# Performance work log

Hardware: AMD Instinct MI355X
Metric: run time of the kernel (lower is better)

Reference implementation:

```python
import jax, jax.numpy as jnp
import numpy as np

EPS = 1e-8  # epsilon from padded_softmax


def setup_inputs() -> dict:
    key = jax.random.key(0)
    k1, k2 = jax.random.split(key)
    B, N, NC = 32, 1024, 3
    C = jax.random.normal(k1, (B, N, NC), dtype=jnp.float32)
    masks = jnp.ones((B, N, N), dtype=jnp.float32)
    # nn.Parameter(torch.rand(1) * 0.02 + 0.99)
    inverse_sigma = jax.random.uniform(k2, (1,), dtype=jnp.float32) * 0.02 + 0.99
    return {"C": C, "masks": masks, "inverse_sigma": inverse_sigma}


def reference(C, masks, inverse_sigma):
    # Pairwise squared euclidean distances via the Gram-matrix identity
    # ||x-y||^2 = ||x||^2 + ||y||^2 - 2<x,y>  (avoids the [B,N,N,NC] expand).
    sq = jnp.sum(C * C, axis=-1)                                  # [B, N]
    gram = jnp.einsum('bnc,bmc->bnm', C, C)                       # [B, N, N]
    D = sq[:, :, None] + sq[:, None, :] - 2.0 * gram              # [B, N, N]
    # Gaussian kernel adjacency.
    A = jnp.exp(-(inverse_sigma ** 2) * D)                        # [B, N, N]
    # padded_softmax: exp(-A) * masks, normalized along last axis.
    X = jnp.exp(-A) * masks
    return X / (jnp.sum(X, axis=-1, keepdims=True) + EPS)
```

## Files before the change

### kernel.cpp

```cpp
#include <hip/hip_runtime.h>

#define EPS 1e-8f
#define LOG2E 1.4426950408889634f

typedef float f32x4 __attribute__((ext_vector_type(4)));

__global__ __launch_bounds__(256) void gaussian_rownorm_kernel(
    const float* __restrict__ C,
    const float* __restrict__ masks,
    const float* __restrict__ inv_sigma,
    float* __restrict__ out,
    int N)
{
    const int n   = blockIdx.x;
    const int b   = blockIdx.y;
    const int t   = threadIdx.x;

    const float s  = inv_sigma[0];
    const float k1 = -(s * s) * LOG2E;

    const float* __restrict__ Cb = C + (size_t)b * N * 3;

    const float cn0 = Cb[n * 3 + 0];
    const float cn1 = Cb[n * 3 + 1];
    const float cn2 = Cb[n * 3 + 2];
    const float sqn = cn0 * cn0 + cn1 * cn1 + cn2 * cn2;

    const int m0 = t * 4;
    const f32x4* __restrict__ cm = (const f32x4*)(Cb + (size_t)m0 * 3);
    const f32x4 ca  = cm[0];
    const f32x4 cb4 = cm[1];
    const f32x4 cc  = cm[2];

    const size_t rowbase = ((size_t)b * N + n) * N;
    const f32x4 mk = __builtin_nontemporal_load((const f32x4*)(masks + rowbase + m0));

    #define CALC(c0, c1, c2, mval)                                   \
        ({                                                           \
            float _sqm = (c0)*(c0) + (c1)*(c1) + (c2)*(c2);          \
            float _dot = cn0*(c0) + cn1*(c1) + cn2*(c2);             \
            float _D   = sqn + _sqm - 2.0f * _dot;                   \
            float _A   = __builtin_amdgcn_exp2f(k1 * _D);            \
            __builtin_amdgcn_exp2f(-LOG2E * _A) * (mval);            \
        })

    const float x0 = CALC(ca.x,  ca.y,  ca.z,  mk.x);
    const float x1 = CALC(ca.w,  cb4.x, cb4.y, mk.y);
    const float x2 = CALC(cb4.z, cb4.w, cc.x,  mk.z);
    const float x3 = CALC(cc.y,  cc.z,  cc.w,  mk.w);
    #undef CALC

    float psum = (x0 + x1) + (x2 + x3);
    #pragma unroll
    for (int off = 32; off > 0; off >>= 1)
        psum += __shfl_xor(psum, off, 64);

    __shared__ float wsum[4];
    const int wid = t >> 6;
    if ((t & 63) == 0) wsum[wid] = psum;
    __syncthreads();

    const float total = wsum[0] + wsum[1] + wsum[2] + wsum[3];
    const float r = 1.0f / (total + EPS);

    f32x4 o;
    o.x = x0 * r; o.y = x1 * r; o.z = x2 * r; o.w = x3 * r;
    __builtin_nontemporal_store(o, (f32x4*)(out + rowbase + m0));
}

extern "C" void kernel_launch(void* const* d_in, const int* in_sizes, int n_in,
                              void* d_out, int out_size, void* d_ws, size_t ws_size,
                              hipStream_t stream) {
    const float* C         = (const float*)d_in[0];
    const float* masks     = (const float*)d_in[1];
    const float* inv_sigma = (const float*)d_in[2];
    float* out             = (float*)d_out;

    const long long N_ll = (long long)out_size * 3LL / (long long)in_sizes[0];
    const int N = (int)N_ll;
    const int B = in_sizes[0] / (3 * N);

    const int block = N / 4;
    dim3 grid(N, B);

    gaussian_rownorm_kernel<<<grid, block, 0, stream>>>(C, masks, inv_sigma, out, N);
}
```

Baseline: 231.0 us.

## Map one wavefront per row for N=1024 to drop block-level reduction

Adds a specialized kernel for N=1024 in which each 64-lane wavefront handles a whole row, with each lane processing 16 elements. The row sum is then done with wavefront shuffles only, removing the shared-memory write and __syncthreads, and each block covers four rows, which cuts the block count by four. All four mask loads are issued up front to raise memory-level parallelism. The trade-off is more registers per thread and a shape-specialized path, with the old kernel kept as a fallback for other sizes.

```diff
diff --git a/kernel.cpp b/kernel.cpp
--- a/kernel.cpp
+++ b/kernel.cpp
@@ -5,22 +5,92 @@
 
 typedef float f32x4 __attribute__((ext_vector_type(4)));
 
-__global__ __launch_bounds__(256) void gaussian_rownorm_kernel(
+#define CALC(c0, c1, c2, mval, cn0, cn1, cn2, sqn, k1)           \
+    ({                                                           \
+        float _sqm = (c0)*(c0) + (c1)*(c1) + (c2)*(c2);          \
+        float _dot = (cn0)*(c0) + (cn1)*(c1) + (cn2)*(c2);       \
+        float _D   = (sqn) + _sqm - 2.0f * _dot;                 \
+        float _A   = __builtin_amdgcn_exp2f((k1) * _D);          \
+        __builtin_amdgcn_exp2f(-LOG2E * _A) * (mval);            \
+    })
+
+__global__ __launch_bounds__(256) void gaussian_rownorm_1024(
+    const float* __restrict__ C,
+    const float* __restrict__ masks,
+    const float* __restrict__ inv_sigma,
+    float* __restrict__ out)
+{
+    constexpr int N = 1024;
+    const int wid  = threadIdx.x >> 6;
+    const int lane = threadIdx.x & 63;
+    const int row  = blockIdx.x * 4 + wid;
+    const int b    = row >> 10;
+    const int n    = row & (N - 1);
+
+    const float s  = inv_sigma[0];
+    const float k1 = -(s * s) * LOG2E;
+
+    const float* __restrict__ Cb = C + (size_t)b * N * 3;
+    const float cn0 = Cb[n * 3 + 0];
+    const float cn1 = Cb[n * 3 + 1];
+    const float cn2 = Cb[n * 3 + 2];
+    const float sqn = cn0 * cn0 + cn1 * cn1 + cn2 * cn2;
+
+    const size_t rowbase = (size_t)row * N;
+
+    f32x4 mk[4];
+    #pragma unroll
+    for (int k = 0; k < 4; ++k)
+        mk[k] = __builtin_nontemporal_load(
+            (const f32x4*)(masks + rowbase + k * 256 + lane * 4));
+
+    float x[16];
+    float psum = 0.0f;
+    #pragma unroll
+    for (int k = 0; k < 4; ++k) {
+        const int m0 = k * 256 + lane * 4;
+        const f32x4* __restrict__ cm = (const f32x4*)(Cb + m0 * 3);
+        const f32x4 ca  = cm[0];
+        const f32x4 cb4 = cm[1];
+        const f32x4 cc  = cm[2];
+
+        x[k*4+0] = CALC(ca.x,  ca.y,  ca.z,  mk[k].x, cn0, cn1, cn2, sqn, k1);
+        x[k*4+1] = CALC(ca.w,  cb4.x, cb4.y, mk[k].y, cn0, cn1, cn2, sqn, k1);
+        x[k*4+2] = CALC(cb4.z, cb4.w, cc.x,  mk[k].z, cn0, cn1, cn2, sqn, k1);
+        x[k*4+3] = CALC(cc.y,  cc.z,  cc.w,  mk[k].w, cn0, cn1, cn2, sqn, k1);
+        psum += (x[k*4+0] + x[k*4+1]) + (x[k*4+2] + x[k*4+3]);
+    }
+
+    #pragma unroll
+    for (int off = 32; off > 0; off >>= 1)
+        psum += __shfl_xor(psum, off, 64);
+
+    const float r = 1.0f / (psum + EPS);
+
+    #pragma unroll
+    for (int k = 0; k < 4; ++k) {
+        f32x4 o;
+        o.x = x[k*4+0] * r; o.y = x[k*4+1] * r;
+        o.z = x[k*4+2] * r; o.w = x[k*4+3] * r;
+        __builtin_nontemporal_store(o, (f32x4*)(out + rowbase + k * 256 + lane * 4));
+    }
+}
+
+__global__ __launch_bounds__(256) void gaussian_rownorm_generic(
     const float* __restrict__ C,
     const float* __restrict__ masks,
     const float* __restrict__ inv_sigma,
     float* __restrict__ out,
     int N)
 {
-    const int n   = blockIdx.x;
-    const int b   = blockIdx.y;
-    const int t   = threadIdx.x;
+    const int n = blockIdx.x;
+    const int b = blockIdx.y;
+    const int t = threadIdx.x;
 
     const float s  = inv_sigma[0];
     const float k1 = -(s * s) * LOG2E;
 
     const float* __restrict__ Cb = C + (size_t)b * N * 3;
-
     const float cn0 = Cb[n * 3 + 0];
     const float cn1 = Cb[n * 3 + 1];
     const float cn2 = Cb[n * 3 + 2];
@@ -35,20 +105,10 @@
     const size_t rowbase = ((size_t)b * N + n) * N;
     const f32x4 mk = __builtin_nontemporal_load((const f32x4*)(masks + rowbase + m0));
 
-    #define CALC(c0, c1, c2, mval)                                   \
-        ({                                                           \
-            float _sqm = (c0)*(c0) + (c1)*(c1) + (c2)*(c2);          \
-            float _dot = cn0*(c0) + cn1*(c1) + cn2*(c2);             \
-            float _D   = sqn + _sqm - 2.0f * _dot;                   \
-            float _A   = __builtin_amdgcn_exp2f(k1 * _D);            \
-            __builtin_amdgcn_exp2f(-LOG2E * _A) * (mval);            \
-        })
-
-    const float x0 = CALC(ca.x,  ca.y,  ca.z,  mk.x);
-    const float x1 = CALC(ca.w,  cb4.x, cb4.y, mk.y);
-    const float x2 = CALC(cb4.z, cb4.w, cc.x,  mk.z);
-    const float x3 = CALC(cc.y,  cc.z,  cc.w,  mk.w);
-    #undef CALC
+    const float x0 = CALC(ca.x,  ca.y,  ca.z,  mk.x, cn0, cn1, cn2, sqn, k1);
+    const float x1 = CALC(ca.w,  cb4.x, cb4.y, mk.y, cn0, cn1, cn2, sqn, k1);
+    const float x2 = CALC(cb4.z, cb4.w, cc.x,  mk.z, cn0, cn1, cn2, sqn, k1);
+    const float x3 = CALC(cc.y,  cc.z,  cc.w,  mk.w, cn0, cn1, cn2, sqn, k1);
 
     float psum = (x0 + x1) + (x2 + x3);
     #pragma unroll
@@ -80,8 +140,11 @@
     const int N = (int)N_ll;
     const int B = in_sizes[0] / (3 * N);
 
-    const int block = N / 4;
-    dim3 grid(N, B);
-
-    gaussian_rownorm_kernel<<<grid, block, 0, stream>>>(C, masks, inv_sigma, out, N);
+    if (N == 1024 && (B * N) % 4 == 0) {
+        const int grid = B * N / 4;
+        gaussian_rownorm_1024<<<grid, 256, 0, stream>>>(C, masks, inv_sigma, out);
+    } else {
+        dim3 grid(N, B);
+        gaussian_rownorm_generic<<<grid, N / 4, 0, stream>>>(C, masks, inv_sigma, out, N);
+    }
 }
```

After: 233.0 us. No clear change (+0.9%).
